# Kernel optimization log

Measured on AMD Instinct MI355X. Metric: run time of the kernel, lower is better.

## Reference

```python
import jax, jax.numpy as jnp
import numpy as np

B, T, D_IN, D, KS = 8, 2048, 64, 512, 3
N_LAYERS = 6
TOP_P = 0.25


def _causal_conv(x, w, b, dil):
    # x: [B, C_in, T], w: [C_out, C_in, K] -> [B, C_out, T]
    pad = (w.shape[-1] - 1) * dil
    y = jax.lax.conv_general_dilated(
        x, w, window_strides=(1,), padding=[(pad, 0)], rhs_dilation=(dil,),
        dimension_numbers=('NCH', 'OIH', 'NCH'))
    return y + b[None, :, None]


def setup_inputs() -> dict:
    key = jax.random.key(0)
    ks = jax.random.split(key, 20)
    s = 0.02
    inp = {
        'x': jax.random.normal(ks[0], (B, T, D_IN), jnp.float32),
        # block 0 (d_in=64 -> d_model=512, dilation 1) + 1x1 residual
        'c1w0': jax.random.normal(ks[1], (D, D_IN, KS), jnp.float32) * s,
        'c1b0': jnp.zeros((D,), jnp.float32),
        'c2w0': jax.random.normal(ks[2], (D, D, KS), jnp.float32) * s,
        'c2b0': jnp.zeros((D,), jnp.float32),
        'resw': jax.random.normal(ks[3], (D, D_IN, 1), jnp.float32) * s,
        'resb': jnp.zeros((D,), jnp.float32),
        # blocks 1..5 stacked (512 -> 512, dilations 2,4,8,16,32), identity residual
        'c1w': jax.random.normal(ks[4], (N_LAYERS - 1, D, D, KS), jnp.float32) * s,
        'c1b': jnp.zeros((N_LAYERS - 1, D), jnp.float32),
        'c2w': jax.random.normal(ks[5], (N_LAYERS - 1, D, D, KS), jnp.float32) * s,
        'c2b': jnp.zeros((N_LAYERS - 1, D), jnp.float32),
        # attention projections (torch Linear: y = x @ W.T + b, W [out,in])
        'wq': jax.random.normal(ks[6], (D, D), jnp.float32) * s,
        'bq': jnp.zeros((D,), jnp.float32),
        'wk': jax.random.normal(ks[7], (D, D), jnp.float32) * s,
        'bk': jnp.zeros((D,), jnp.float32),
        'wv': jax.random.normal(ks[8], (D, D), jnp.float32) * s,
        'bv': jnp.zeros((D,), jnp.float32),
        'wp': jax.random.normal(ks[9], (D, D), jnp.float32) * s,
        'bp': jnp.zeros((D,), jnp.float32),
    }
    return inp


def _forward(x, c1w0, c1b0, c2w0, c2b0, resw, resb, c1w, c1b, c2w, c2b,
             wq, bq, wk, bk, wv, bv, wp, bp):
    gelu = lambda t: jax.nn.gelu(t, approximate=False)
    h = jnp.swapaxes(x, 1, 2)  # [B, D_IN, T]
    # block 0 with 1x1-conv residual (d_in != d_out)
    y = gelu(_causal_conv(h, c1w0, c1b0, 1))
    y = gelu(_causal_conv(y, c2w0, c2b0, 1))
    h = y + _causal_conv(h, resw, resb, 1)
    # blocks 1..5, identity residual
    for i in range(N_LAYERS - 1):
        dil = 2 ** (i + 1)
        y = gelu(_causal_conv(h, c1w[i], c1b[i], dil))
        y = gelu(_causal_conv(y, c2w[i], c2b[i], dil))
        h = y + h
    z = jnp.swapaxes(h, 1, 2)  # [B, T, D]

    # sparse top-p attention
    q = z @ wq.T + bq
    k = z @ wk.T + bk
    v = z @ wv.T + bv
    scores = jnp.einsum('bqd,bkd->bqk', q, k) / jnp.sqrt(jnp.float32(D))
    k_keep = max(1, int(TOP_P * T))
    vals, idx = jax.lax.top_k(scores, k_keep)  # [B, T, k_keep]
    neg_inf = jnp.array(-jnp.inf, scores.dtype)
    mask = jnp.full_like(scores, neg_inf)
    b_ix = jnp.arange(B)[:, None, None]
    t_ix = jnp.arange(T)[None, :, None]
    mask = mask.at[b_ix, t_ix, idx].set(vals)
    attn = jax.nn.softmax(mask, axis=-1)
    attn_out = jnp.einsum('bqk,bkd->bqd', attn, v)[:, -1, :]  # [B, D]

    return (z[:, -1, :] + attn_out) @ wp.T + bp


def reference(x, c1w0, c1b0, c2w0, c2b0, resw, resb, c1w, c1b, c2w, c2b,
              wq, bq, wk, bk, wv, bv, wp, bp):
    return _forward(x, c1w0, c1b0, c2w0, c2b0, resw, resb, c1w, c1b, c2w, c2b,
                    wq, bq, wk, bk, wv, bv, wp, bp)
```

## Files before the change

### kernel.cpp

```cpp
#include <hip/hip_runtime.h>
#include <hip/hip_bf16.h>
#include <math.h>

#define B_ 8
#define T_ 2048
#define PT_ 2112
#define DIN_ 64
#define D_ 512

typedef __attribute__((ext_vector_type(8))) short bf16x8;
typedef __attribute__((ext_vector_type(4))) float f32x4;

#define HROW(b, t) (((size_t)(b) * PT_ + 64 + (t)) * D_)

__device__ __forceinline__ float gelu_f(float x) {
    return 0.5f * x * (1.0f + erff(x * 0.70710678118654752440f));
}
__device__ __forceinline__ float bfu2f(unsigned short u) {
    union { float f; unsigned int i; } v; v.i = ((unsigned int)u) << 16; return v.f;
}
__device__ __forceinline__ unsigned short f2bf(float f) {
    unsigned int x = __float_as_uint(f);
    return (unsigned short)((x + 0x7FFFu + ((x >> 16) & 1u)) >> 16);
}
__device__ __forceinline__ void gload_lds16(const void* g, void* l) {
    __builtin_amdgcn_global_load_lds(
        (const __attribute__((address_space(1))) void*)g,
        (__attribute__((address_space(3))) void*)l, 16, 0, 0);
}

__global__ __launch_bounds__(256) void k_setup(const float* __restrict__ x,
                                               unsigned short* __restrict__ xb,
                                               unsigned short* bufA,
                                               unsigned short* bufB) {
    const int NX = B_ * 64 * DIN_;
    const int NA = B_ * 64 * D_;
    const int NC = B_ * T_ * DIN_;
    int i = blockIdx.x * 256 + threadIdx.x;
    if (i < NX) {
        const int b = i / (64 * DIN_), r = i - b * (64 * DIN_);
        xb[(size_t)b * PT_ * DIN_ + r] = 0;
        return;
    }
    i -= NX;
    if (i < NA) {
        const int b = i / (64 * D_), r = i - b * (64 * D_);
        bufA[(size_t)b * PT_ * D_ + r] = 0;
        return;
    }
    i -= NA;
    if (i < NA) {
        const int b = i / (64 * D_), r = i - b * (64 * D_);
        bufB[(size_t)b * PT_ * D_ + r] = 0;
        return;
    }
    i -= NA;
    if (i < NC) {
        const int b = i / (T_ * DIN_);
        const int r = i - b * (T_ * DIN_);
        xb[((size_t)b * PT_ + 64) * DIN_ + r] = f2bf(x[i]);
    }
}

__global__ __launch_bounds__(256) void k_wcvt_all(const float* resw, const float* c1w0,
                                                  const float* c2w0, const float* c1w,
                                                  const float* c2w,
                                                  unsigned short* wRes, unsigned short* wC10,
                                                  unsigned short* wC20, unsigned short* wC1,
                                                  unsigned short* wC2) {
    const int l = blockIdx.y;
    const float* src;
    unsigned short* dst;
    int C_in, KS;
    if (l == 0)      { src = resw; dst = wRes; C_in = 64;  KS = 1; }
    else if (l == 1) { src = c1w0; dst = wC10; C_in = 64;  KS = 3; }
    else if (l == 2) { src = c2w0; dst = wC20; C_in = 512; KS = 3; }
    else if (l <= 7) { src = c1w + (size_t)(l - 3) * 512 * 512 * 3;
                       dst = wC1 + (size_t)(l - 3) * 3 * 512 * 512; C_in = 512; KS = 3; }
    else             { src = c2w + (size_t)(l - 8) * 512 * 512 * 3;
                       dst = wC2 + (size_t)(l - 8) * 3 * 512 * 512; C_in = 512; KS = 3; }
    const int n = 512 * C_in * KS;
    for (int i = blockIdx.x * 256 + threadIdx.x; i < n; i += gridDim.x * 256) {
        const int ci = i % C_in;
        const int r = i / C_in;
        const int co = r & 511;
        const int tap = r >> 9;
        dst[i] = f2bf(src[((size_t)co * C_in + ci) * KS + tap]);
    }
}

template <int KS, int MODE>
__global__ __launch_bounds__(256, 2) void k_conv_mfma(const unsigned short* __restrict__ X,
                                                      const unsigned short* __restrict__ Wt,
                                                      const float* __restrict__ bias,
                                                      const unsigned short* R,
                                                      unsigned short* Y,
                                                      int C_in, int dil) {
    const int tid = threadIdx.x;
    const int ib = blockIdx.x;
    const int work = (ib & 7) * 8 + (ib >> 3);
    const int co0 = (work & 3) * 128;
    const int t0 = (work >> 2) * 128;
    const int b = blockIdx.z;
    const int back = (KS - 1) * dil;
    const int XWIN = 128 + back;

    __shared__ __align__(16) unsigned short sX[192 * 64];
    __shared__ __align__(16) unsigned short sW[KS * 128 * 64];

    const int lane = tid & 63;
    const int wv = tid >> 6;
    const int wco = (wv & 1) * 64;
    const int wt = (wv >> 1) * 64;
    const int tl = lane & 15;
    const int ch = lane >> 4;

    f32x4 acc[4][4] = {};

    const unsigned short* Xb = X + ((size_t)b * PT_ + 64) * C_in;

    const unsigned short* xsrc[6];
#pragma unroll
    for (int k = 0; k < 6; ++k) {
        const int i = tid + k * 256;
        const int row = i >> 3, s = i & 7;
        int tg = t0 - back + row;
        if (tg >= T_) tg = T_ - 1;
        xsrc[k] = Xb + (size_t)tg * C_in + ((s ^ (row & 7)) << 3);
    }
    const unsigned short* wsrc[KS * 4];
#pragma unroll
    for (int k = 0; k < KS * 4; ++k) {
        const int i = tid + k * 256;
        const int row = i >> 3, s = i & 7;
        const int tap = row >> 7, rco = row & 127;
        wsrc[k] = Wt + ((size_t)(tap * 512 + co0 + rco)) * C_in + ((s ^ (row & 7)) << 3);
    }
    const int nx = XWIN * 8;

    const int NC = C_in >> 6;
    for (int c = 0; c < NC; ++c) {
        if (c) __syncthreads();
#pragma unroll
        for (int k = 0; k < 6; ++k) {
            const int i = tid + k * 256;
            if (i < nx) gload_lds16(xsrc[k] + c * 64, &sX[(i & ~63) * 8]);
        }
#pragma unroll
        for (int k = 0; k < KS * 4; ++k) {
            const int i = tid + k * 256;
            gload_lds16(wsrc[k] + c * 64, &sW[(i & ~63) * 8]);
        }
        __syncthreads();

#pragma unroll
        for (int tap = 0; tap < KS; ++tap) {
            const int tapoff = tap * dil;
#pragma unroll
            for (int ks = 0; ks < 2; ++ks) {
                const int j = ks * 4 + ch;
                bf16x8 a[4], bb[4];
#pragma unroll
                for (int m = 0; m < 4; ++m) {
                    const int wr = tap * 128 + wco + m * 16 + tl;
                    a[m] = *reinterpret_cast<const bf16x8*>(
                        &sW[wr * 64 + ((j ^ (wr & 7)) << 3)]);
                }
#pragma unroll
                for (int n = 0; n < 4; ++n) {
                    const int xr = wt + n * 16 + tl + tapoff;
                    bb[n] = *reinterpret_cast<const bf16x8*>(
                        &sX[xr * 64 + ((j ^ (xr & 7)) << 3)]);
                }
#pragma unroll
                for (int m = 0; m < 4; ++m)
#pragma unroll
                    for (int n = 0; n < 4; ++n)
                        acc[m][n] = __builtin_amdgcn_mfma_f32_16x16x32_bf16(a[m], bb[n], acc[m][n], 0, 0, 0);
            }
        }
    }

#pragma unroll
    for (int m = 0; m < 4; ++m) {
        const int co = co0 + wco + m * 16 + ch * 4;
        const float4 bv4 = *reinterpret_cast<const float4*>(&bias[co]);
#pragma unroll
        for (int n = 0; n < 4; ++n) {
            const int t = t0 + wt + n * 16 + tl;
            const size_t base = HROW(b, t) + co;
            float v[4];
            v[0] = acc[m][n][0] + bv4.x;
            v[1] = acc[m][n][1] + bv4.y;
            v[2] = acc[m][n][2] + bv4.z;
            v[3] = acc[m][n][3] + bv4.w;
            if (MODE >= 1) {
#pragma unroll
                for (int r = 0; r < 4; ++r) v[r] = gelu_f(v[r]);
            }
            if (MODE == 2) {
                const uint2 rr = *reinterpret_cast<const uint2*>(&R[base]);
                v[0] += bfu2f((unsigned short)(rr.x & 0xffffu));
                v[1] += bfu2f((unsigned short)(rr.x >> 16));
                v[2] += bfu2f((unsigned short)(rr.y & 0xffffu));
                v[3] += bfu2f((unsigned short)(rr.y >> 16));
            }
            uint2 o;
            o.x = (unsigned int)f2bf(v[0]) | ((unsigned int)f2bf(v[1]) << 16);
            o.y = (unsigned int)f2bf(v[2]) | ((unsigned int)f2bf(v[3]) << 16);
            *reinterpret_cast<uint2*>(&Y[base]) = o;
        }
    }
}

__global__ __launch_bounds__(256) void k_q(const unsigned short* __restrict__ h,
                                           const float* __restrict__ wq,
                                           const float* __restrict__ bq,
                                           float* __restrict__ q) {
    __shared__ float zs[B_ * D_];
    const int tid = threadIdx.x;
    for (int i = tid; i < B_ * D_; i += 256) {
        const int b = i >> 9, c = i & 511;
        zs[i] = bfu2f(h[HROW(b, T_ - 1) + c]);
    }
    __syncthreads();
    const int wvi = tid >> 6, lane = tid & 63;
    const int d = blockIdx.x * 4 + wvi;
    const float* wr = wq + (size_t)d * D_ + lane * 8;
    float w8[8];
#pragma unroll
    for (int j = 0; j < 8; ++j) w8[j] = wr[j];
    float acc[B_];
#pragma unroll
    for (int b = 0; b < B_; ++b) {
        float a = 0.0f;
#pragma unroll
        for (int j = 0; j < 8; ++j) a += w8[j] * zs[b * D_ + lane * 8 + j];
        acc[b] = a;
    }
#pragma unroll
    for (int off = 32; off; off >>= 1) {
#pragma unroll
        for (int b = 0; b < B_; ++b) acc[b] += __shfl_xor(acc[b], off);
    }
    if (lane == 0) {
#pragma unroll
        for (int b = 0; b < B_; ++b) q[b * D_ + d] = acc[b] + bq[d];
    }
}

__global__ __launch_bounds__(512) void k_qk(const float* __restrict__ q,
                                            const float* __restrict__ wk,
                                            const float* __restrict__ bk,
                                            float* __restrict__ qkvec,
                                            float* __restrict__ qbk) {
    const int b = blockIdx.y, dc = blockIdx.x;
    const int tid = threadIdx.x;
    __shared__ float qs[64];
    if (tid < 64) qs[tid] = q[b * D_ + dc * 64 + tid];
    __syncthreads();
    float acc = 0.0f;
    const float* wbase = wk + (size_t)(dc * 64) * D_ + tid;
#pragma unroll 8
    for (int d = 0; d < 64; ++d) acc += qs[d] * wbase[(size_t)d * D_];
    atomicAdd(&qkvec[b * D_ + tid], acc);
    if (tid < 64) {
        float p = qs[tid] * bk[dc * 64 + tid];
#pragma unroll
        for (int off = 32; off; off >>= 1) p += __shfl_xor(p, off);
        if (tid == 0) atomicAdd(&qbk[b], p);
    }
}

__global__ __launch_bounds__(256) void k_scores(const unsigned short* __restrict__ h,
                                                const float* __restrict__ qkvec,
                                                const float* __restrict__ qbk,
                                                float* __restrict__ scores) {
    const int b = blockIdx.y;
    const int tid = threadIdx.x;
    __shared__ float qs[D_];
    qs[tid] = qkvec[b * D_ + tid];
    qs[tid + 256] = qkvec[b * D_ + tid + 256];
    __syncthreads();
    const int wvi = tid >> 6, lane = tid & 63;
    const int t = blockIdx.x * 4 + wvi;
    const uint4 v = *reinterpret_cast<const uint4*>(h + HROW(b, t) + lane * 8);
    const unsigned int w[4] = {v.x, v.y, v.z, v.w};
    float acc = 0.0f;
#pragma unroll
    for (int j = 0; j < 4; ++j) {
        acc += bfu2f((unsigned short)(w[j] & 0xffffu)) * qs[lane * 8 + 2 * j];
        acc += bfu2f((unsigned short)(w[j] >> 16)) * qs[lane * 8 + 2 * j + 1];
    }
    for (int off = 32; off; off >>= 1) acc += __shfl_down(acc, off);
    if (lane == 0) scores[b * T_ + t] = (acc + qbk[b]) * 0.04419417382415922f;
}

__global__ __launch_bounds__(1024) void k_topk(const float* __restrict__ scores,
                                               float* __restrict__ wts) {
    const int b = blockIdx.x;
    __shared__ float s[T_];
    __shared__ float v[T_];
    __shared__ float red[16];
    __shared__ float denom_s;
    for (int i = threadIdx.x; i < T_; i += 1024) {
        const float x = scores[b * T_ + i];
        s[i] = x; v[i] = x;
    }
    __syncthreads();
    for (unsigned kk = 2; kk <= T_; kk <<= 1) {
        for (unsigned j = kk >> 1; j > 0; j >>= 1) {
            for (unsigned i = threadIdx.x; i < T_; i += 1024) {
                const unsigned ixj = i ^ j;
                if (ixj > i) {
                    const float a = v[i], c2 = v[ixj];
                    const bool asc = ((i & kk) == 0);
                    if ((a > c2) == asc) { v[i] = c2; v[ixj] = a; }
                }
            }
            __syncthreads();
        }
    }
    const float thr = v[T_ - 512];
    const float mx = v[T_ - 1];
    float part = 0.0f;
    for (int i = threadIdx.x; i < T_; i += 1024) {
        const float x = s[i];
        if (x >= thr) part += expf(x - mx);
    }
    for (int off = 32; off; off >>= 1) part += __shfl_down(part, off);
    const int lane = threadIdx.x & 63, wv_ = threadIdx.x >> 6;
    if (lane == 0) red[wv_] = part;
    __syncthreads();
    if (threadIdx.x == 0) {
        float d = 0.0f;
        for (int i = 0; i < 16; ++i) d += red[i];
        denom_s = d;
    }
    __syncthreads();
    const float inv = 1.0f / denom_s;
    for (int i = threadIdx.x; i < T_; i += 1024) {
        const float x = s[i];
        wts[b * T_ + i] = (x >= thr) ? expf(x - mx) * inv : 0.0f;
    }
}

__global__ __launch_bounds__(256) void k_zv(const unsigned short* __restrict__ h,
                                            const float* __restrict__ wts,
                                            float* __restrict__ zvb) {
    const int b = blockIdx.y;
    const int t0 = blockIdx.x * 256;
    const int tid = threadIdx.x;
    float a0 = 0.0f, a1 = 0.0f;
    for (int t = t0; t < t0 + 256; ++t) {
        const float w = wts[b * T_ + t];
        if (w != 0.0f) {
            const unsigned int v = *reinterpret_cast<const unsigned int*>(
                h + HROW(b, t) + tid * 2);
            a0 += w * bfu2f((unsigned short)(v & 0xffffu));
            a1 += w * bfu2f((unsigned short)(v >> 16));
        }
    }
    atomicAdd(&zvb[b * D_ + tid * 2], a0);
    atomicAdd(&zvb[b * D_ + tid * 2 + 1], a1);
}

__global__ __launch_bounds__(256) void k_u(const unsigned short* __restrict__ h,
                                           const float* __restrict__ zvb,
                                           const float* __restrict__ wv,
                                           const float* __restrict__ bv,
                                           float* __restrict__ u) {
    __shared__ float zs[B_ * D_];
    const int tid = threadIdx.x;
    for (int i = tid; i < B_ * D_; i += 256) zs[i] = zvb[i];
    __syncthreads();
    const int wvi = tid >> 6, lane = tid & 63;
    const int e = blockIdx.x * 4 + wvi;
    const float* wr = wv + (size_t)e * D_ + lane * 8;
    float w8[8];
#pragma unroll
    for (int j = 0; j < 8; ++j) w8[j] = wr[j];
    float acc[B_];
#pragma unroll
    for (int b = 0; b < B_; ++b) {
        float a = 0.0f;
#pragma unroll
        for (int j = 0; j < 8; ++j) a += w8[j] * zs[b * D_ + lane * 8 + j];
        acc[b] = a;
    }
#pragma unroll
    for (int off = 32; off; off >>= 1) {
#pragma unroll
        for (int b = 0; b < B_; ++b) acc[b] += __shfl_xor(acc[b], off);
    }
    if (lane == 0) {
#pragma unroll
        for (int b = 0; b < B_; ++b)
            u[b * D_ + e] = acc[b] + bv[e] + bfu2f(h[HROW(b, T_ - 1) + e]);
    }
}

__global__ __launch_bounds__(256) void k_out(const float* __restrict__ u,
                                             const float* __restrict__ wp,
                                             const float* __restrict__ bp,
                                             float* __restrict__ out) {
    __shared__ float us[B_ * D_];
    const int tid = threadIdx.x;
    for (int i = tid; i < B_ * D_; i += 256) us[i] = u[i];
    __syncthreads();
    const int wvi = tid >> 6, lane = tid & 63;
    const int d = blockIdx.x * 4 + wvi;
    const float* wr = wp + (size_t)d * D_ + lane * 8;
    float w8[8];
#pragma unroll
    for (int j = 0; j < 8; ++j) w8[j] = wr[j];
    float acc[B_];
#pragma unroll
    for (int b = 0; b < B_; ++b) {
        float a = 0.0f;
#pragma unroll
        for (int j = 0; j < 8; ++j) a += w8[j] * us[b * D_ + lane * 8 + j];
        acc[b] = a;
    }
#pragma unroll
    for (int off = 32; off; off >>= 1) {
#pragma unroll
        for (int b = 0; b < B_; ++b) acc[b] += __shfl_xor(acc[b], off);
    }
    if (lane == 0) {
#pragma unroll
        for (int b = 0; b < B_; ++b) out[b * D_ + d] = acc[b] + bp[d];
    }
}

extern "C" void kernel_launch(void* const* d_in, const int* in_sizes, int n_in,
                              void* d_out, int out_size, void* d_ws, size_t ws_size,
                              hipStream_t stream) {
    const float* x    = (const float*)d_in[0];
    const float* c1w0 = (const float*)d_in[1];
    const float* c1b0 = (const float*)d_in[2];
    const float* c2w0 = (const float*)d_in[3];
    const float* c2b0 = (const float*)d_in[4];
    const float* resw = (const float*)d_in[5];
    const float* resb = (const float*)d_in[6];
    const float* c1w  = (const float*)d_in[7];
    const float* c1b  = (const float*)d_in[8];
    const float* c2w  = (const float*)d_in[9];
    const float* c2b  = (const float*)d_in[10];
    const float* wq   = (const float*)d_in[11];
    const float* bq   = (const float*)d_in[12];
    const float* wk   = (const float*)d_in[13];
    const float* bk   = (const float*)d_in[14];
    const float* wvp  = (const float*)d_in[15];
    const float* bv   = (const float*)d_in[16];
    const float* wp   = (const float*)d_in[17];
    const float* bp   = (const float*)d_in[18];
    float* out = (float*)d_out;

    unsigned short* ws16 = (unsigned short*)d_ws;
    unsigned short* xb   = ws16;
    unsigned short* bufA = xb + (size_t)B_ * PT_ * DIN_;
    unsigned short* bufB = bufA + (size_t)B_ * PT_ * D_;
    unsigned short* wRes = bufB + (size_t)B_ * PT_ * D_;
    unsigned short* wC10 = wRes + 512 * 64;
    unsigned short* wC20 = wC10 + 3 * 512 * 64;
    unsigned short* wC1  = wC20 + 3 * 512 * 512;
    unsigned short* wC2  = wC1 + (size_t)5 * 3 * 512 * 512;
    float* fws  = (float*)(wC2 + (size_t)5 * 3 * 512 * 512);
    float* qv    = fws;
    float* qkvec = qv + B_ * D_;
    float* qbk   = qkvec + B_ * D_;
    float* zvb   = qbk + 8;
    float* uacc  = zvb + B_ * D_;
    float* sc    = uacc + B_ * D_;
    float* wts   = sc + B_ * T_;

    const int nsetup = B_ * 64 * (DIN_ + 2 * D_) + B_ * T_ * DIN_;
    k_setup<<<dim3((nsetup + 255) / 256), 256, 0, stream>>>(x, xb, bufA, bufB);
    k_wcvt_all<<<dim3(768, 13), 256, 0, stream>>>(resw, c1w0, c2w0, c1w, c2w,
                                                  wRes, wC10, wC20, wC1, wC2);
    hipMemsetAsync(qkvec, 0, (2 * B_ * D_ + 8) * sizeof(float), stream);

    const dim3 cgrid(64, 1, B_);
    k_conv_mfma<1, 0><<<cgrid, 256, 0, stream>>>(xb, wRes, resb, nullptr, bufA, DIN_, 1);
    k_conv_mfma<3, 1><<<cgrid, 256, 0, stream>>>(xb, wC10, c1b0, nullptr, bufB, DIN_, 1);
    k_conv_mfma<3, 2><<<cgrid, 256, 0, stream>>>(bufB, wC20, c2b0, bufA, bufA, D_, 1);
    for (int i = 0; i < 5; ++i) {
        const int dil = 2 << i;
        k_conv_mfma<3, 1><<<cgrid, 256, 0, stream>>>(bufA, wC1 + (size_t)i * 3 * 512 * 512,
                                                     c1b + i * D_, nullptr, bufB, D_, dil);
        k_conv_mfma<3, 2><<<cgrid, 256, 0, stream>>>(bufB, wC2 + (size_t)i * 3 * 512 * 512,
                                                     c2b + i * D_, bufA, bufA, D_, dil);
    }

    k_q<<<128, 256, 0, stream>>>(bufA, wq, bq, qv);
    k_qk<<<dim3(8, 8), 512, 0, stream>>>(qv, wk, bk, qkvec, qbk);
    k_scores<<<dim3(T_ / 4, B_), 256, 0, stream>>>(bufA, qkvec, qbk, sc);
    k_topk<<<B_, 1024, 0, stream>>>(sc, wts);
    k_zv<<<dim3(T_ / 256, B_), 256, 0, stream>>>(bufA, wts, zvb);
    k_u<<<128, 256, 0, stream>>>(bufA, zvb, wvp, bv, uacc);
    k_out<<<128, 256, 0, stream>>>(uacc, wp, bp, out);
}
```

Baseline: 458.4 us.

## Fuse block-0 convs and tail matvec kernels; drop memset and intermediate launches

Combines the 1x1 residual conv and the first dilated conv of block 0 into one launch, with a y-dimension selecting which one each block computes. Fuses the q projection with the q·Wk product into one per-batch kernel, and the value projection with the output projection into another. Folds the zvb zeroing into the setup kernel, which removes the memset and the atomics on qkvec/qbk. Fewer launches and less round-tripping through global memory are traded for the tail kernels running on only 8 blocks, so each weight matrix is reread per batch with little parallelism.

```diff
diff --git a/kernel.cpp b/kernel.cpp
--- a/kernel.cpp
+++ b/kernel.cpp
@@ -32,10 +32,12 @@
 __global__ __launch_bounds__(256) void k_setup(const float* __restrict__ x,
                                                unsigned short* __restrict__ xb,
                                                unsigned short* bufA,
-                                               unsigned short* bufB) {
+                                               unsigned short* bufB,
+                                               float* zvb) {
     const int NX = B_ * 64 * DIN_;
     const int NA = B_ * 64 * D_;
     const int NC = B_ * T_ * DIN_;
+    const int NZ = B_ * D_;
     int i = blockIdx.x * 256 + threadIdx.x;
     if (i < NX) {
         const int b = i / (64 * DIN_), r = i - b * (64 * DIN_);
@@ -59,7 +61,10 @@
         const int b = i / (T_ * DIN_);
         const int r = i - b * (T_ * DIN_);
         xb[((size_t)b * PT_ + 64) * DIN_ + r] = f2bf(x[i]);
-    }
+        return;
+    }
+    i -= NC;
+    if (i < NZ) zvb[i] = 0.0f;
 }
 
 __global__ __launch_bounds__(256) void k_wcvt_all(const float* resw, const float* c1w0,
@@ -89,6 +94,109 @@
     }
 }
 
+__global__ __launch_bounds__(256, 2) void k_conv_b0(const unsigned short* __restrict__ X,
+                                                    const unsigned short* __restrict__ wRes,
+                                                    const float* __restrict__ resb,
+                                                    const unsigned short* __restrict__ wC10,
+                                                    const float* __restrict__ c1b0,
+                                                    unsigned short* bufA,
+                                                    unsigned short* bufB) {
+    const int tid = threadIdx.x;
+    const int ib = blockIdx.x;
+    const int work = (ib & 7) * 8 + (ib >> 3);
+    const int co0 = (work & 3) * 128;
+    const int t0 = (work >> 2) * 128;
+    const int b = blockIdx.z;
+    const int y = blockIdx.y;
+    const int nks = y ? 3 : 1;
+    const unsigned short* Wt = y ? wC10 : wRes;
+    const float* bias = y ? c1b0 : resb;
+    unsigned short* Y = y ? bufB : bufA;
+    const int back = nks - 1;
+    const int nx = (128 + back) * 8;
+
+    __shared__ __align__(16) unsigned short sX[192 * 64];
+    __shared__ __align__(16) unsigned short sW[3 * 128 * 64];
+
+    const int lane = tid & 63;
+    const int wv = tid >> 6;
+    const int wco = (wv & 1) * 64;
+    const int wt = (wv >> 1) * 64;
+    const int tl = lane & 15;
+    const int ch = lane >> 4;
+
+    f32x4 acc[4][4] = {};
+
+    const unsigned short* Xb = X + ((size_t)b * PT_ + 64) * DIN_;
+
+#pragma unroll
+    for (int k = 0; k < 6; ++k) {
+        const int i = tid + k * 256;
+        if (i < nx) {
+            const int row = i >> 3, s = i & 7;
+            int tg = t0 - back + row;
+            if (tg >= T_) tg = T_ - 1;
+            gload_lds16(Xb + (size_t)tg * DIN_ + ((s ^ (row & 7)) << 3), &sX[(i & ~63) * 8]);
+        }
+    }
+    for (int k = 0; k < nks * 4; ++k) {
+        const int i = tid + k * 256;
+        const int row = i >> 3, s = i & 7;
+        const int tap = row >> 7, rco = row & 127;
+        gload_lds16(Wt + ((size_t)(tap * 512 + co0 + rco)) * DIN_ + ((s ^ (row & 7)) << 3),
+                    &sW[(i & ~63) * 8]);
+    }
+    __syncthreads();
+
+    for (int tap = 0; tap < nks; ++tap) {
+        const int tapoff = tap;
+#pragma unroll
+        for (int kh = 0; kh < 2; ++kh) {
+            const int j = kh * 4 + ch;
+            bf16x8 a[4], bb[4];
+#pragma unroll
+            for (int m = 0; m < 4; ++m) {
+                const int wr = tap * 128 + wco + m * 16 + tl;
+                a[m] = *reinterpret_cast<const bf16x8*>(&sW[wr * 64 + ((j ^ (wr & 7)) << 3)]);
+            }
+#pragma unroll
+            for (int n = 0; n < 4; ++n) {
+                const int xr = wt + n * 16 + tl + tapoff;
+                bb[n] = *reinterpret_cast<const bf16x8*>(&sX[xr * 64 + ((j ^ (xr & 7)) << 3)]);
+            }
+#pragma unroll
+            for (int m = 0; m < 4; ++m)
+#pragma unroll
+                for (int n = 0; n < 4; ++n)
+                    acc[m][n] = __builtin_amdgcn_mfma_f32_16x16x32_bf16(a[m], bb[n], acc[m][n], 0, 0, 0);
+        }
+    }
+
+#pragma unroll
+    for (int m = 0; m < 4; ++m) {
+        const int co = co0 + wco + m * 16 + ch * 4;
+        const float4 bv4 = *reinterpret_cast<const float4*>(&bias[co]);
+#pragma unroll
+        for (int n = 0; n < 4; ++n) {
+            const int t = t0 + wt + n * 16 + tl;
+            const size_t base = HROW(b, t) + co;
+            float v[4];
+            v[0] = acc[m][n][0] + bv4.x;
+            v[1] = acc[m][n][1] + bv4.y;
+            v[2] = acc[m][n][2] + bv4.z;
+            v[3] = acc[m][n][3] + bv4.w;
+            if (y) {
+#pragma unroll
+                for (int r = 0; r < 4; ++r) v[r] = gelu_f(v[r]);
+            }
+            uint2 o;
+            o.x = (unsigned int)f2bf(v[0]) | ((unsigned int)f2bf(v[1]) << 16);
+            o.y = (unsigned int)f2bf(v[2]) | ((unsigned int)f2bf(v[3]) << 16);
+            *reinterpret_cast<uint2*>(&Y[base]) = o;
+        }
+    }
+}
+
 template <int KS, int MODE>
 __global__ __launch_bounds__(256, 2) void k_conv_mfma(const unsigned short* __restrict__ X,
                                                       const unsigned short* __restrict__ Wt,
@@ -213,62 +321,45 @@
     }
 }
 
-__global__ __launch_bounds__(256) void k_q(const unsigned short* __restrict__ h,
-                                           const float* __restrict__ wq,
-                                           const float* __restrict__ bq,
-                                           float* __restrict__ q) {
-    __shared__ float zs[B_ * D_];
-    const int tid = threadIdx.x;
-    for (int i = tid; i < B_ * D_; i += 256) {
-        const int b = i >> 9, c = i & 511;
-        zs[i] = bfu2f(h[HROW(b, T_ - 1) + c]);
-    }
-    __syncthreads();
-    const int wvi = tid >> 6, lane = tid & 63;
-    const int d = blockIdx.x * 4 + wvi;
-    const float* wr = wq + (size_t)d * D_ + lane * 8;
-    float w8[8];
-#pragma unroll
-    for (int j = 0; j < 8; ++j) w8[j] = wr[j];
-    float acc[B_];
-#pragma unroll
-    for (int b = 0; b < B_; ++b) {
+__global__ __launch_bounds__(512) void k_qfused(const unsigned short* __restrict__ h,
+                                                const float* __restrict__ wq,
+                                                const float* __restrict__ bq,
+                                                const float* __restrict__ wk,
+                                                const float* __restrict__ bk,
+                                                float* __restrict__ qkvec,
+                                                float* __restrict__ qbk) {
+    const int b = blockIdx.x, tid = threadIdx.x;
+    const int lane = tid & 63, wv = tid >> 6;
+    __shared__ float zl[D_];
+    __shared__ float qs[D_];
+    __shared__ float red[8];
+    if (tid < D_) zl[tid] = bfu2f(h[HROW(b, T_ - 1) + tid]);
+    __syncthreads();
+    for (int k = 0; k < 64; ++k) {
+        const int d = wv * 64 + k;
+        const float* row = wq + (size_t)d * D_ + lane * 8;
         float a = 0.0f;
 #pragma unroll
-        for (int j = 0; j < 8; ++j) a += w8[j] * zs[b * D_ + lane * 8 + j];
-        acc[b] = a;
-    }
-#pragma unroll
-    for (int off = 32; off; off >>= 1) {
-#pragma unroll
-        for (int b = 0; b < B_; ++b) acc[b] += __shfl_xor(acc[b], off);
-    }
-    if (lane == 0) {
-#pragma unroll
-        for (int b = 0; b < B_; ++b) q[b * D_ + d] = acc[b] + bq[d];
-    }
-}
-
-__global__ __launch_bounds__(512) void k_qk(const float* __restrict__ q,
-                                            const float* __restrict__ wk,
-                                            const float* __restrict__ bk,
-                                            float* __restrict__ qkvec,
-                                            float* __restrict__ qbk) {
-    const int b = blockIdx.y, dc = blockIdx.x;
-    const int tid = threadIdx.x;
-    __shared__ float qs[64];
-    if (tid < 64) qs[tid] = q[b * D_ + dc * 64 + tid];
+        for (int j = 0; j < 8; ++j) a += row[j] * zl[lane * 8 + j];
+#pragma unroll
+        for (int off = 32; off; off >>= 1) a += __shfl_xor(a, off);
+        if (lane == 0) qs[d] = a + bq[d];
+    }
     __syncthreads();
     float acc = 0.0f;
-    const float* wbase = wk + (size_t)(dc * 64) * D_ + tid;
 #pragma unroll 8
-    for (int d = 0; d < 64; ++d) acc += qs[d] * wbase[(size_t)d * D_];
-    atomicAdd(&qkvec[b * D_ + tid], acc);
-    if (tid < 64) {
-        float p = qs[tid] * bk[dc * 64 + tid];
-#pragma unroll
-        for (int off = 32; off; off >>= 1) p += __shfl_xor(p, off);
-        if (tid == 0) atomicAdd(&qbk[b], p);
+    for (int d = 0; d < D_; ++d) acc += qs[d] * wk[(size_t)d * D_ + tid];
+    qkvec[b * D_ + tid] = acc;
+    float p = qs[tid] * bk[tid];
+#pragma unroll
+    for (int off = 32; off; off >>= 1) p += __shfl_xor(p, off);
+    if (lane == 0) red[wv] = p;
+    __syncthreads();
+    if (tid == 0) {
+        float s = 0.0f;
+#pragma unroll
+        for (int i = 0; i < 8; ++i) s += red[i];
+        qbk[b] = s;
     }
 }
 
@@ -365,71 +456,39 @@
     atomicAdd(&zvb[b * D_ + tid * 2 + 1], a1);
 }
 
-__global__ __launch_bounds__(256) void k_u(const unsigned short* __restrict__ h,
-                                           const float* __restrict__ zvb,
-                                           const float* __restrict__ wv,
-                                           const float* __restrict__ bv,
-                                           float* __restrict__ u) {
-    __shared__ float zs[B_ * D_];
-    const int tid = threadIdx.x;
-    for (int i = tid; i < B_ * D_; i += 256) zs[i] = zvb[i];
-    __syncthreads();
-    const int wvi = tid >> 6, lane = tid & 63;
-    const int e = blockIdx.x * 4 + wvi;
-    const float* wr = wv + (size_t)e * D_ + lane * 8;
-    float w8[8];
-#pragma unroll
-    for (int j = 0; j < 8; ++j) w8[j] = wr[j];
-    float acc[B_];
-#pragma unroll
-    for (int b = 0; b < B_; ++b) {
+__global__ __launch_bounds__(512) void k_ufused(const unsigned short* __restrict__ h,
+                                                const float* __restrict__ zvb,
+                                                const float* __restrict__ wv,
+                                                const float* __restrict__ bv,
+                                                const float* __restrict__ wp,
+                                                const float* __restrict__ bp,
+                                                float* __restrict__ out) {
+    const int b = blockIdx.x, tid = threadIdx.x;
+    const int lane = tid & 63, wvi = tid >> 6;
+    __shared__ float zvs[D_];
+    __shared__ float us[D_];
+    if (tid < D_) zvs[tid] = zvb[b * D_ + tid];
+    __syncthreads();
+    for (int k = 0; k < 64; ++k) {
+        const int e = wvi * 64 + k;
+        const float* row = wv + (size_t)e * D_ + lane * 8;
         float a = 0.0f;
 #pragma unroll
-        for (int j = 0; j < 8; ++j) a += w8[j] * zs[b * D_ + lane * 8 + j];
-        acc[b] = a;
-    }
-#pragma unroll
-    for (int off = 32; off; off >>= 1) {
-#pragma unroll
-        for (int b = 0; b < B_; ++b) acc[b] += __shfl_xor(acc[b], off);
-    }
-    if (lane == 0) {
-#pragma unroll
-        for (int b = 0; b < B_; ++b)
-            u[b * D_ + e] = acc[b] + bv[e] + bfu2f(h[HROW(b, T_ - 1) + e]);
-    }
-}
-
-__global__ __launch_bounds__(256) void k_out(const float* __restrict__ u,
-                                             const float* __restrict__ wp,
-                                             const float* __restrict__ bp,
-                                             float* __restrict__ out) {
-    __shared__ float us[B_ * D_];
-    const int tid = threadIdx.x;
-    for (int i = tid; i < B_ * D_; i += 256) us[i] = u[i];
-    __syncthreads();
-    const int wvi = tid >> 6, lane = tid & 63;
-    const int d = blockIdx.x * 4 + wvi;
-    const float* wr = wp + (size_t)d * D_ + lane * 8;
-    float w8[8];
-#pragma unroll
-    for (int j = 0; j < 8; ++j) w8[j] = wr[j];
-    float acc[B_];
-#pragma unroll
-    for (int b = 0; b < B_; ++b) {
+        for (int j = 0; j < 8; ++j) a += row[j] * zvs[lane * 8 + j];
+#pragma unroll
+        for (int off = 32; off; off >>= 1) a += __shfl_xor(a, off);
+        if (lane == 0) us[e] = a + bv[e] + bfu2f(h[HROW(b, T_ - 1) + e]);
+    }
+    __syncthreads();
+    for (int k = 0; k < 64; ++k) {
+        const int d = wvi * 64 + k;
+        const float* row = wp + (size_t)d * D_ + lane * 8;
         float a = 0.0f;
 #pragma unroll
-        for (int j = 0; j < 8; ++j) a += w8[j] * us[b * D_ + lane * 8 + j];
-        acc[b] = a;
-    }
-#pragma unroll
-    for (int off = 32; off; off >>= 1) {
-#pragma unroll
-        for (int b = 0; b < B_; ++b) acc[b] += __shfl_xor(acc[b], off);
-    }
-    if (lane == 0) {
-#pragma unroll
-        for (int b = 0; b < B_; ++b) out[b * D_ + d] = acc[b] + bp[d];
+        for (int j = 0; j < 8; ++j) a += row[j] * us[lane * 8 + j];
+#pragma unroll
+        for (int off = 32; off; off >>= 1) a += __shfl_xor(a, off);
+        if (lane == 0) out[b * D_ + d] = a + bp[d];
     }
 }
 
@@ -467,23 +526,19 @@
     unsigned short* wC1  = wC20 + 3 * 512 * 512;
     unsigned short* wC2  = wC1 + (size_t)5 * 3 * 512 * 512;
     float* fws  = (float*)(wC2 + (size_t)5 * 3 * 512 * 512);
-    float* qv    = fws;
-    float* qkvec = qv + B_ * D_;
+    float* qkvec = fws;
     float* qbk   = qkvec + B_ * D_;
     float* zvb   = qbk + 8;
-    float* uacc  = zvb + B_ * D_;
-    float* sc    = uacc + B_ * D_;
+    float* sc    = zvb + B_ * D_;
     float* wts   = sc + B_ * T_;
 
-    const int nsetup = B_ * 64 * (DIN_ + 2 * D_) + B_ * T_ * DIN_;
-    k_setup<<<dim3((nsetup + 255) / 256), 256, 0, stream>>>(x, xb, bufA, bufB);
+    const int nsetup = B_ * 64 * (DIN_ + 2 * D_) + B_ * T_ * DIN_ + B_ * D_;
+    k_setup<<<dim3((nsetup + 255) / 256), 256, 0, stream>>>(x, xb, bufA, bufB, zvb);
     k_wcvt_all<<<dim3(768, 13), 256, 0, stream>>>(resw, c1w0, c2w0, c1w, c2w,
                                                   wRes, wC10, wC20, wC1, wC2);
-    hipMemsetAsync(qkvec, 0, (2 * B_ * D_ + 8) * sizeof(float), stream);
 
     const dim3 cgrid(64, 1, B_);
-    k_conv_mfma<1, 0><<<cgrid, 256, 0, stream>>>(xb, wRes, resb, nullptr, bufA, DIN_, 1);
-    k_conv_mfma<3, 1><<<cgrid, 256, 0, stream>>>(xb, wC10, c1b0, nullptr, bufB, DIN_, 1);
+    k_conv_b0<<<dim3(64, 2, B_), 256, 0, stream>>>(xb, wRes, resb, wC10, c1b0, bufA, bufB);
     k_conv_mfma<3, 2><<<cgrid, 256, 0, stream>>>(bufB, wC20, c2b0, bufA, bufA, D_, 1);
     for (int i = 0; i < 5; ++i) {
         const int dil = 2 << i;
@@ -493,11 +548,9 @@
                                                      c2b + i * D_, bufA, bufA, D_, dil);
     }
 
-    k_q<<<128, 256, 0, stream>>>(bufA, wq, bq, qv);
-    k_qk<<<dim3(8, 8), 512, 0, stream>>>(qv, wk, bk, qkvec, qbk);
+    k_qfused<<<B_, 512, 0, stream>>>(bufA, wq, bq, wk, bk, qkvec, qbk);
     k_scores<<<dim3(T_ / 4, B_), 256, 0, stream>>>(bufA, qkvec, qbk, sc);
     k_topk<<<B_, 1024, 0, stream>>>(sc, wts);
     k_zv<<<dim3(T_ / 256, B_), 256, 0, stream>>>(bufA, wts, zvb);
-    k_u<<<128, 256, 0, stream>>>(bufA, zvb, wvp, bv, uacc);
-    k_out<<<128, 256, 0, stream>>>(uacc, wp, bp, out);
-}
+    k_ufused<<<B_, 512, 0, stream>>>(bufA, zvb, wvp, bv, wp, bp, out);
+}
```

Result: slower. 594.6 us (+29.7%).
